# Kernel tuning notes

Hardware: AMD Instinct MI355X
Metric: run time of the kernel (lower is better)

## Reference

```python
import jax, jax.numpy as jnp
import numpy as np

N_NODES = 50000
N_EDGES = 800000
IN_DIM = 128
HID = 128
NUM_CLASSES = 2


def setup_inputs() -> dict:
    key = jax.random.key(0)
    ks = jax.random.split(key, 16)
    inp = {
        "adj_row": jax.random.randint(ks[0], (N_EDGES,), 0, N_NODES),
        "adj_col": jax.random.randint(ks[1], (N_EDGES,), 0, N_NODES),
        "adj_vals": jax.random.uniform(ks[2], (N_EDGES,), dtype=jnp.float32),
        "input_feature": jax.random.normal(ks[3], (N_NODES, IN_DIM), dtype=jnp.float32),
        "graph_indicator": jax.random.randint(ks[4], (N_NODES,), 0, 64),
        # GCN layer params (kaiming-uniform-ish init; zeros bias like the torch module)
        "W1": jax.random.uniform(ks[5], (IN_DIM, HID), jnp.float32, -1, 1) * np.sqrt(6.0 / IN_DIM),
        "b1": jnp.zeros((HID,), jnp.float32),
        "W2": jax.random.uniform(ks[6], (HID, HID), jnp.float32, -1, 1) * np.sqrt(6.0 / HID),
        "b2": jnp.zeros((HID,), jnp.float32),
        "W3": jax.random.uniform(ks[7], (HID, HID), jnp.float32, -1, 1) * np.sqrt(6.0 / HID),
        "b3": jnp.zeros((HID,), jnp.float32),
        # fc params (torch.nn.Linear default init range)
        "fcW1": jax.random.uniform(ks[8], (3 * HID, HID), jnp.float32, -1, 1) / np.sqrt(3 * HID),
        "fcb1": jax.random.uniform(ks[9], (HID,), jnp.float32, -1, 1) / np.sqrt(3 * HID),
        "fcW2": jax.random.uniform(ks[10], (HID, HID // 2), jnp.float32, -1, 1) / np.sqrt(HID),
        "fcb2": jax.random.uniform(ks[11], (HID // 2,), jnp.float32, -1, 1) / np.sqrt(HID),
        "fcW3": jax.random.uniform(ks[12], (HID // 2, NUM_CLASSES), jnp.float32, -1, 1) / np.sqrt(HID // 2),
        "fcb3": jax.random.uniform(ks[13], (NUM_CLASSES,), jnp.float32, -1, 1) / np.sqrt(HID // 2),
    }
    return inp


def _gcn_layer(row, col, vals, x, W, b, n_nodes):
    # support = X @ W  -> dense GEMM
    support = x @ W
    # sparse.mm(A, support): out[i] = sum_{e: row[e]=i} vals[e] * support[col[e]]
    msgs = support[col] * vals[:, None]  # [E, D] gather + scale
    agg = jax.ops.segment_sum(msgs, row, num_segments=n_nodes)
    return agg + b


def reference(adj_row, adj_col, adj_vals, input_feature, graph_indicator,
              W1, b1, W2, b2, W3, b3, fcW1, fcb1, fcW2, fcb2, fcW3, fcb3):
    n = input_feature.shape[0]
    g1 = jax.nn.relu(_gcn_layer(adj_row, adj_col, adj_vals, input_feature, W1, b1, n))
    g2 = jax.nn.relu(_gcn_layer(adj_row, adj_col, adj_vals, g1, W2, b2, n))
    g3 = jax.nn.relu(_gcn_layer(adj_row, adj_col, adj_vals, g2, W3, b3, n))
    feat = jnp.concatenate([g1, g2, g3], axis=1)  # [N, 3*HID]
    h = jax.nn.relu(feat @ fcW1 + fcb1)
    h = jax.nn.relu(h @ fcW2 + fcb2)
    logits = h @ fcW3 + fcb3
    return logits
```

## Files before the change

kernel.cpp:

```cpp
#include <hip/hip_runtime.h>
#include <hip/hip_bf16.h>

#define N_NODES 50000
#define N_EDGES 800000
#define NBK 391
#define BCAP 2560
#define PADSLACK 896

static inline int cdiv(int a, int b) { return (a + b - 1) / b; }

typedef __attribute__((ext_vector_type(8))) short short8;
typedef __attribute__((ext_vector_type(4))) float f32x4;

__device__ __forceinline__ float b2f(unsigned short u) {
    union { unsigned int i; float f; } c;
    c.i = ((unsigned int)u) << 16;
    return c.f;
}
__device__ __forceinline__ unsigned short f2bb(float f) {
    __hip_bfloat16 h = __float2bfloat16(f);
    return *(unsigned short*)&h;
}

__device__ __forceinline__ void pack_one(const float* __restrict__ W,
                                         __hip_bfloat16* __restrict__ out,
                                         int K, int N, int t) {
    int lane = t & 63;
    int kc = (t >> 6) % (K / 32);
    int nt = (t >> 6) / (K / 32);
    int kbase = kc * 32 + (lane >> 4) * 8;
    int col = nt * 16 + (lane & 15);
    __hip_bfloat16* dst = out + (size_t)t * 8;
#pragma unroll
    for (int j = 0; j < 8; ++j)
        dst[j] = __float2bfloat16(W[(size_t)(kbase + j) * N + col]);
}

__global__ __launch_bounds__(256)
void stage1_kernel(const int* __restrict__ row, const int* __restrict__ col,
                   const float* __restrict__ vals, int* __restrict__ bcursor,
                   int2* __restrict__ tmp, int E,
                   const float* __restrict__ x, __hip_bfloat16* __restrict__ support,
                   int M,
                   const float* __restrict__ W1, const float* __restrict__ W2,
                   const float* __restrict__ W3, const float* __restrict__ fcW1,
                   const float* __restrict__ fcW2,
                   __hip_bfloat16* __restrict__ pW2, __hip_bfloat16* __restrict__ pW3,
                   __hip_bfloat16* __restrict__ pfcW1, __hip_bfloat16* __restrict__ pfcW2) {
    __shared__ unsigned short As[64][136];
    __shared__ int hist[NBK];
    __shared__ int base[NBK];
    const int b = blockIdx.x;
    const int tid = threadIdx.x;

    if (b < 196) {
        const int CH = 4096;
        int e0 = b * CH;
        for (int i = tid; i < NBK; i += 256) hist[i] = 0;
        __syncthreads();
        for (int i = tid; i < CH; i += 256) {
            int e = e0 + i;
            if (e < E) atomicAdd(&hist[row[e] >> 7], 1);
        }
        __syncthreads();
        for (int i = tid; i < NBK; i += 256) {
            int c = hist[i];
            base[i] = (c > 0) ? (i * BCAP + atomicAdd(&bcursor[i], c)) : 0;
            hist[i] = 0;
        }
        __syncthreads();
        for (int i = tid; i < CH; i += 256) {
            int e = e0 + i;
            if (e < E) {
                int r = row[e];
                int bk = r >> 7;
                int rk = atomicAdd(&hist[bk], 1);
                tmp[base[bk] + rk] = make_int2(((r & 127) << 16) | col[e],
                                               __float_as_int(vals[e]));
            }
        }
        return;
    }

    if (b < 978) {
        const int wave = tid >> 6;
        const int lane = tid & 63;
        const int ln15 = lane & 15;
        const int quad = lane >> 4;
        const int m0 = (b - 196) * 64;

        short8 bfr[4][2];
#pragma unroll
        for (int kc = 0; kc < 4; ++kc)
#pragma unroll
            for (int h = 0; h < 2; ++h)
#pragma unroll
                for (int j = 0; j < 8; ++j)
                    bfr[kc][h][j] = (short)f2bb(
                        W1[(size_t)(kc * 32 + quad * 8 + j) * 128 + (wave * 2 + h) * 16 + ln15]);

#pragma unroll
        for (int i = 0; i < 4; ++i) {
            int idx = tid + i * 256;
            int r = idx >> 4;
            int c8 = (idx & 15) * 8;
            uint4 pk = {0, 0, 0, 0};
            if (m0 + r < M) {
                const float* src = &x[(size_t)(m0 + r) * 128 + c8];
                float4 a = *(const float4*)src;
                float4 bq = *(const float4*)(src + 4);
                pk.x = f2bb(a.x) | ((unsigned int)f2bb(a.y) << 16);
                pk.y = f2bb(a.z) | ((unsigned int)f2bb(a.w) << 16);
                pk.z = f2bb(bq.x) | ((unsigned int)f2bb(bq.y) << 16);
                pk.w = f2bb(bq.z) | ((unsigned int)f2bb(bq.w) << 16);
            }
            *(uint4*)&As[r][c8] = pk;
        }
        __syncthreads();

        f32x4 acc[4][2];
#pragma unroll
        for (int s = 0; s < 4; ++s)
#pragma unroll
            for (int h = 0; h < 2; ++h) acc[s][h] = (f32x4){0.f, 0.f, 0.f, 0.f};
#pragma unroll
        for (int kc = 0; kc < 4; ++kc) {
            short8 af[4];
#pragma unroll
            for (int s = 0; s < 4; ++s)
                af[s] = *(const short8*)&As[s * 16 + ln15][kc * 32 + quad * 8];
#pragma unroll
            for (int s = 0; s < 4; ++s)
#pragma unroll
                for (int h = 0; h < 2; ++h)
                    acc[s][h] = __builtin_amdgcn_mfma_f32_16x16x32_bf16(
                        af[s], bfr[kc][h], acc[s][h], 0, 0, 0);
        }
#pragma unroll
        for (int s = 0; s < 4; ++s)
#pragma unroll
            for (int h = 0; h < 2; ++h) {
                int cl = (wave * 2 + h) * 16 + ln15;
#pragma unroll
                for (int r = 0; r < 4; ++r) {
                    int rw = m0 + s * 16 + quad * 4 + r;
                    if (rw < M)
                        support[(size_t)rw * 128 + cl] = __float2bfloat16(acc[s][h][r]);
                }
            }
        return;
    }

    int pb = b - 978;
    if (pb < 8)       pack_one(W2,  pW2,  128, 128, pb * 256 + tid);
    else if (pb < 16) pack_one(W3,  pW3,  128, 128, (pb - 8) * 256 + tid);
    else if (pb < 40) pack_one(fcW1, pfcW1, 384, 128, (pb - 16) * 256 + tid);
    else              pack_one(fcW2, pfcW2, 128, 64, (pb - 40) * 256 + tid);
}

__global__ __launch_bounds__(256)
void binB_kernel(const int2* __restrict__ tmp, const int* __restrict__ bcursor,
                 int2* __restrict__ rowrange, int2* __restrict__ epack, int N) {
    int b = blockIdx.x;
    int r0 = b << 7;
    int nr = N - r0; if (nr > 128) nr = 128;
    __shared__ int cnt[128];
    __shared__ int cur[128];
    __shared__ int rpos[128];
    __shared__ int red[256];
    int t = threadIdx.x;
    int partial = 0;
    for (int i = t; i < b; i += 256) partial += bcursor[i];
    red[t] = partial;
    if (t < 128) cnt[t] = 0;
    __syncthreads();
    for (int off = 128; off > 0; off >>= 1) {
        if (t < off) red[t] += red[t + off];
        __syncthreads();
    }
    int slab = b * BCAP;
    int send = slab + bcursor[b];
    for (int i = slab + t; i < send; i += 256)
        atomicAdd(&cnt[tmp[i].x >> 16], 1);
    __syncthreads();
    int rcnt = (t < 128) ? cnt[t] : 0;
    int pc = (rcnt + 7) & ~7;
    if (t < 128) cur[t] = pc;
    __syncthreads();
    for (int off = 1; off < 128; off <<= 1) {
        int u = (t >= off && t < 128) ? cur[t - off] : 0;
        __syncthreads();
        if (t < 128) cur[t] += u;
        __syncthreads();
    }
    int obase = red[0] + b * PADSLACK;
    if (t < 128) {
        int pos = obase + cur[t] - pc;
        rpos[t] = pos;
        cur[t] = pos;
        if (t < nr) rowrange[r0 + t] = make_int2(pos, pos + pc);
    }
    __syncthreads();
    for (int i = slab + t; i < send; i += 256) {
        int2 v = tmp[i];
        int rl = v.x >> 16;
        int c = v.x & 0xffff;
        int pos = atomicAdd(&cur[rl], 1);
        epack[pos] = make_int2(c, v.y);
    }
    if (t < 128) {
        int rc = rcnt;
        int pos = rpos[t];
#pragma unroll 1
        for (int i = pos + rc; i < pos + pc; ++i)
            epack[i] = make_int2(0, 0);
    }
}

__device__ __forceinline__ void accum8(float* acc, long long e, uint4 u) {
    float f = __int_as_float((int)(e >> 32));
    acc[0] += f * b2f((unsigned short)(u.x & 0xffff));
    acc[1] += f * b2f((unsigned short)(u.x >> 16));
    acc[2] += f * b2f((unsigned short)(u.y & 0xffff));
    acc[3] += f * b2f((unsigned short)(u.y >> 16));
    acc[4] += f * b2f((unsigned short)(u.z & 0xffff));
    acc[5] += f * b2f((unsigned short)(u.z >> 16));
    acc[6] += f * b2f((unsigned short)(u.w & 0xffff));
    acc[7] += f * b2f((unsigned short)(u.w >> 16));
}

__device__ __forceinline__ void agg_node(const long long* __restrict__ ep,
                                         const __hip_bfloat16* __restrict__ support,
                                         int p, int end, int g, int j, float* acc) {
#pragma unroll
    for (int k = 0; k < 8; ++k) acc[k] = 0.f;
    long long e0 = 0, e1 = 0;
    uint4 u0 = {0, 0, 0, 0}, u1 = {0, 0, 0, 0};
    bool have = false;
    if (p < end) {
        e0 = ep[p + g];
        e1 = ep[p + 4 + g];
        u0 = *(const uint4*)&support[(size_t)(unsigned int)(e0 & 0xffffffffu) * 128 + j * 8];
        u1 = *(const uint4*)&support[(size_t)(unsigned int)(e1 & 0xffffffffu) * 128 + j * 8];
        p += 8;
        have = true;
    }
    while (p < end) {
        long long f0 = ep[p + g];
        long long f1 = ep[p + 4 + g];
        uint4 w0 = *(const uint4*)&support[(size_t)(unsigned int)(f0 & 0xffffffffu) * 128 + j * 8];
        uint4 w1 = *(const uint4*)&support[(size_t)(unsigned int)(f1 & 0xffffffffu) * 128 + j * 8];
        accum8(acc, e0, u0);
        accum8(acc, e1, u1);
        e0 = f0; u0 = w0; e1 = f1; u1 = w1;
        p += 8;
    }
    if (have) {
        accum8(acc, e0, u0);
        accum8(acc, e1, u1);
    }
#pragma unroll
    for (int k = 0; k < 8; ++k) {
        acc[k] += __shfl_xor(acc[k], 16);
        acc[k] += __shfl_xor(acc[k], 32);
    }
}

__global__ __launch_bounds__(256, 3)
void spmm_gemm_kernel(const int2* __restrict__ rowrange,
                      const int2* __restrict__ epack,
                      const __hip_bfloat16* __restrict__ support,
                      const float* __restrict__ bias,
                      __hip_bfloat16* __restrict__ gout,
                      const __hip_bfloat16* __restrict__ pW,
                      __hip_bfloat16* __restrict__ Cout,
                      int N) {
    __shared__ unsigned short As[64][136];
    const int tid = threadIdx.x;
    const int wv = tid >> 6;
    const int l = tid & 63;
    const int g = l >> 4;
    const int j = l & 15;
    const int m0 = blockIdx.x * 64;
    const long long* ep = (const long long*)epack;
    float4 b0 = *(const float4*)&bias[j * 8];
    float4 b1 = *(const float4*)&bias[j * 8 + 4];

    for (int i = 0; i < 16; ++i) {
        int node = m0 + wv * 16 + i;
        if (node >= N) {
            if (g == 0) *(uint4*)&As[wv * 16 + i][j * 8] = (uint4){0, 0, 0, 0};
            continue;
        }
        int2 rr = rowrange[node];
        float acc[8];
        agg_node(ep, support, rr.x, rr.y, g, j, acc);
        if (g == 0) {
            unsigned int q0 = (unsigned int)f2bb(fmaxf(acc[0] + b0.x, 0.f))
                            | ((unsigned int)f2bb(fmaxf(acc[1] + b0.y, 0.f)) << 16);
            unsigned int q1 = (unsigned int)f2bb(fmaxf(acc[2] + b0.z, 0.f))
                            | ((unsigned int)f2bb(fmaxf(acc[3] + b0.w, 0.f)) << 16);
            unsigned int q2 = (unsigned int)f2bb(fmaxf(acc[4] + b1.x, 0.f))
                            | ((unsigned int)f2bb(fmaxf(acc[5] + b1.y, 0.f)) << 16);
            unsigned int q3 = (unsigned int)f2bb(fmaxf(acc[6] + b1.z, 0.f))
                            | ((unsigned int)f2bb(fmaxf(acc[7] + b1.w, 0.f)) << 16);
            uint4 st = {q0, q1, q2, q3};
            *(uint4*)&As[wv * 16 + i][j * 8] = st;
            *(uint4*)&gout[(size_t)node * 384 + j * 8] = st;
        }
    }
    __syncthreads();

    const int ln15 = l & 15;
    const int quad = l >> 4;
    const int ntw = wv * 2;
    f32x4 acc2[4][2];
#pragma unroll
    for (int s = 0; s < 4; ++s)
#pragma unroll
        for (int h = 0; h < 2; ++h) acc2[s][h] = (f32x4){0.f, 0.f, 0.f, 0.f};
#pragma unroll
    for (int kc = 0; kc < 4; ++kc) {
        short8 af[4];
#pragma unroll
        for (int s = 0; s < 4; ++s)
            af[s] = *(const short8*)&As[s * 16 + ln15][kc * 32 + quad * 8];
        short8 bf[2];
#pragma unroll
        for (int h = 0; h < 2; ++h)
            bf[h] = *(const short8*)&pW[((size_t)((ntw + h) * 4 + kc) * 64 + l) * 8];
#pragma unroll
        for (int s = 0; s < 4; ++s)
#pragma unroll
            for (int h = 0; h < 2; ++h)
                acc2[s][h] = __builtin_amdgcn_mfma_f32_16x16x32_bf16(
                    af[s], bf[h], acc2[s][h], 0, 0, 0);
    }
#pragma unroll
    for (int s = 0; s < 4; ++s)
#pragma unroll
        for (int h = 0; h < 2; ++h) {
            int cl = (ntw + h) * 16 + ln15;
#pragma unroll
            for (int r = 0; r < 4; ++r) {
                int rw = m0 + s * 16 + quad * 4 + r;
                if (rw < N)
                    Cout[(size_t)rw * 128 + cl] = __float2bfloat16(acc2[s][h][r]);
            }
        }
}

__global__ __launch_bounds__(256, 3)
void spmm_fc_kernel(const int2* __restrict__ rowrange,
                    const int2* __restrict__ epack,
                    const __hip_bfloat16* __restrict__ support,
                    const float* __restrict__ bias,
                    const __hip_bfloat16* __restrict__ featb,
                    const __hip_bfloat16* __restrict__ pfcW1,
                    const float* __restrict__ fcb1,
                    const __hip_bfloat16* __restrict__ pfcW2,
                    const float* __restrict__ fcb2,
                    const float* __restrict__ fcW3, const float* __restrict__ fcb3,
                    float* __restrict__ out, int N) {
    __shared__ unsigned short As[64][136];
    __shared__ float w3s[128];
    __shared__ float b3s[2];
    const int tid = threadIdx.x;
    const int wv = tid >> 6;
    const int l = tid & 63;
    const int g = l >> 4;
    const int j = l & 15;
    const int m0 = blockIdx.x * 64;
    const long long* ep = (const long long*)epack;
    if (tid < 128) w3s[tid] = fcW3[tid];
    if (tid < 2) b3s[tid] = fcb3[tid];
    float4 b0 = *(const float4*)&bias[j * 8];
    float4 b1 = *(const float4*)&bias[j * 8 + 4];

    for (int i = 0; i < 16; ++i) {
        int node = m0 + wv * 16 + i;
        if (node >= N) {
            if (g == 0) *(uint4*)&As[wv * 16 + i][j * 8] = (uint4){0, 0, 0, 0};
            continue;
        }
        int2 rr = rowrange[node];
        float acc[8];
        agg_node(ep, support, rr.x, rr.y, g, j, acc);
        if (g == 0) {
            unsigned int q0 = (unsigned int)f2bb(fmaxf(acc[0] + b0.x, 0.f))
                            | ((unsigned int)f2bb(fmaxf(acc[1] + b0.y, 0.f)) << 16);
            unsigned int q1 = (unsigned int)f2bb(fmaxf(acc[2] + b0.z, 0.f))
                            | ((unsigned int)f2bb(fmaxf(acc[3] + b0.w, 0.f)) << 16);
            unsigned int q2 = (unsigned int)f2bb(fmaxf(acc[4] + b1.x, 0.f))
                            | ((unsigned int)f2bb(fmaxf(acc[5] + b1.y, 0.f)) << 16);
            unsigned int q3 = (unsigned int)f2bb(fmaxf(acc[6] + b1.z, 0.f))
                            | ((unsigned int)f2bb(fmaxf(acc[7] + b1.w, 0.f)) << 16);
            uint4 st = {q0, q1, q2, q3};
            *(uint4*)&As[wv * 16 + i][j * 8] = st;
        }
    }
    __syncthreads();

    const int lane = l;
    const int ln15 = lane & 15;
    const int quad = lane >> 4;
    const int wave = wv;
    f32x4 acc[4][2];
#pragma unroll
    for (int s = 0; s < 4; ++s)
#pragma unroll
        for (int h = 0; h < 2; ++h) acc[s][h] = (f32x4){0.f, 0.f, 0.f, 0.f};
#pragma unroll
    for (int step = 0; step < 3; ++step) {
        const int kb = (step == 0) ? 2 : (step - 1);
        if (step != 0) {
            __syncthreads();
#pragma unroll
            for (int i = 0; i < 4; ++i) {
                int idx = tid + i * 256;
                int r = idx >> 4;
                int c8 = (idx & 15) * 8;
                uint4 v = *(const uint4*)&featb[(size_t)(m0 + r) * 384 + kb * 128 + c8];
                *(uint4*)&As[r][c8] = v;
            }
            __syncthreads();
        }
#pragma unroll
        for (int kc = 0; kc < 4; ++kc) {
            short8 af[4];
#pragma unroll
            for (int s = 0; s < 4; ++s)
                af[s] = *(const short8*)&As[s * 16 + ln15][kc * 32 + quad * 8];
            short8 bf[2];
#pragma unroll
            for (int h = 0; h < 2; ++h) {
                int kcg = kb * 4 + kc;
                bf[h] = *(const short8*)&pfcW1[((size_t)((wave * 2 + h) * 12 + kcg) * 64 + lane) * 8];
            }
#pragma unroll
            for (int s = 0; s < 4; ++s)
#pragma unroll
                for (int h = 0; h < 2; ++h)
                    acc[s][h] = __builtin_amdgcn_mfma_f32_16x16x32_bf16(
                        af[s], bf[h], acc[s][h], 0, 0, 0);
        }
    }
    __syncthreads();
#pragma unroll
    for (int s = 0; s < 4; ++s)
#pragma unroll
        for (int h = 0; h < 2; ++h) {
            int col = (wave * 2 + h) * 16 + ln15;
            float bv = fcb1[col];
#pragma unroll
            for (int r = 0; r < 4; ++r) {
                int row = s * 16 + quad * 4 + r;
                As[row][col] = f2bb(fmaxf(acc[s][h][r] + bv, 0.f));
            }
        }
    __syncthreads();

    f32x4 acc2[4];
#pragma unroll
    for (int s = 0; s < 4; ++s) acc2[s] = (f32x4){0.f, 0.f, 0.f, 0.f};
#pragma unroll
    for (int kc = 0; kc < 4; ++kc) {
        short8 af[4];
#pragma unroll
        for (int s = 0; s < 4; ++s)
            af[s] = *(const short8*)&As[s * 16 + ln15][kc * 32 + quad * 8];
        short8 bfw = *(const short8*)&pfcW2[((size_t)(wave * 4 + kc) * 64 + lane) * 8];
#pragma unroll
        for (int s = 0; s < 4; ++s)
            acc2[s] = __builtin_amdgcn_mfma_f32_16x16x32_bf16(af[s], bfw, acc2[s], 0, 0, 0);
    }
    __syncthreads();
    {
        int col2 = wave * 16 + ln15;
        float bv = fcb2[col2];
#pragma unroll
        for (int s = 0; s < 4; ++s)
#pragma unroll
            for (int r = 0; r < 4; ++r) {
                int row = s * 16 + quad * 4 + r;
                As[row][col2] = f2bb(fmaxf(acc2[s][r] + bv, 0.f));
            }
    }
    __syncthreads();

    if (tid < 128) {
        int row = tid >> 1, cls = tid & 1;
        int grow = m0 + row;
        if (grow < N) {
            float a = b3s[cls];
#pragma unroll
            for (int k = 0; k < 64; ++k)
                a += b2f(As[row][k]) * w3s[k * 2 + cls];
            out[(size_t)grow * 2 + cls] = a;
        }
    }
}

extern "C" void kernel_launch(void* const* d_in, const int* in_sizes, int n_in,
                              void* d_out, int out_size, void* d_ws, size_t ws_size,
                              hipStream_t stream) {
    const int*   adj_row  = (const int*)d_in[0];
    const int*   adj_col  = (const int*)d_in[1];
    const float* adj_vals = (const float*)d_in[2];
    const float* x        = (const float*)d_in[3];
    const float* W1   = (const float*)d_in[5];
    const float* b1   = (const float*)d_in[6];
    const float* W2   = (const float*)d_in[7];
    const float* b2   = (const float*)d_in[8];
    const float* W3   = (const float*)d_in[9];
    const float* b3   = (const float*)d_in[10];
    const float* fcW1 = (const float*)d_in[11];
    const float* fcb1 = (const float*)d_in[12];
    const float* fcW2 = (const float*)d_in[13];
    const float* fcb2 = (const float*)d_in[14];
    const float* fcW3 = (const float*)d_in[15];
    const float* fcb3 = (const float*)d_in[16];
    float* out = (float*)d_out;

    const int N = N_NODES, E = N_EDGES;
    const int Mpad = 50048;
    const int EPAD = E + NBK * PADSLACK + 64;

    char* p = (char*)d_ws;
    auto alloc = [&](size_t bytes) {
        char* q = p;
        p += (bytes + 255) & ~(size_t)255;
        return q;
    };
    __hip_bfloat16* featb    = (__hip_bfloat16*)alloc((size_t)Mpad * 384 * 2);
    __hip_bfloat16* supportb = (__hip_bfloat16*)alloc((size_t)Mpad * 128 * 2);
    __hip_bfloat16* supportc = (__hip_bfloat16*)alloc((size_t)Mpad * 128 * 2);
    __hip_bfloat16* pW2   = (__hip_bfloat16*)alloc(16384 * 2);
    __hip_bfloat16* pW3   = (__hip_bfloat16*)alloc(16384 * 2);
    __hip_bfloat16* pfcW1 = (__hip_bfloat16*)alloc(49152 * 2);
    __hip_bfloat16* pfcW2 = (__hip_bfloat16*)alloc(8192 * 2);
    int2*  rowrange  = (int2*)alloc((size_t)(N + 1) * 8);
    int*   bcursor   = (int*)alloc((size_t)NBK * 4);
    int2*  epack     = (int2*)alloc((size_t)EPAD * 8);
    int2*  tmp       = (int2*)alloc((size_t)NBK * BCAP * 8);

    hipMemsetAsync(bcursor, 0, (size_t)NBK * 4, stream);
    stage1_kernel<<<1022, 256, 0, stream>>>(adj_row, adj_col, adj_vals, bcursor, tmp, E,
                                            x, supportb, N,
                                            W1, W2, W3, fcW1, fcW2,
                                            pW2, pW3, pfcW1, pfcW2);
    binB_kernel<<<NBK, 256, 0, stream>>>(tmp, bcursor, rowrange, epack, N);

    const int fgrid = cdiv(N, 64);

    spmm_gemm_kernel<<<fgrid, 256, 0, stream>>>(rowrange, epack, supportb, b1,
                                                featb + 0, pW2, supportc, N);
    spmm_gemm_kernel<<<fgrid, 256, 0, stream>>>(rowrange, epack, supportc, b2,
                                                featb + 128, pW3, supportb, N);
    spmm_fc_kernel<<<fgrid, 256, 0, stream>>>(rowrange, epack, supportb, b3,
                                              featb, pfcW1, fcb1, pfcW2, fcb2,
                                              fcW3, fcb3, out, N);
}
```

Measured before the change: 273.9 us.

## Use 512-thread blocks in fused SpMM kernels, one MFMA tile per wave

The fused aggregation+GEMM kernels now launch 8 waves per 64-node block instead of 4. Each wave aggregates 8 nodes instead of 16 and computes one 16-column output tile instead of two. This raises the number of waves in flight for the latency-bound gather, at the cost of an extra barrier branch and idle waves in the fc2 stage. The fc kernel runs its second layer on only the first four waves. The non-uniform __syncthreads inside the if/else branches is a correctness risk.

```diff
diff --git a/kernel.cpp b/kernel.cpp
--- a/kernel.cpp
+++ b/kernel.cpp
@@ -266,7 +266,7 @@
     }
 }
 
-__global__ __launch_bounds__(256, 3)
+__global__ __launch_bounds__(512, 4)
 void spmm_gemm_kernel(const int2* __restrict__ rowrange,
                       const int2* __restrict__ epack,
                       const __hip_bfloat16* __restrict__ support,
@@ -286,10 +286,10 @@
     float4 b0 = *(const float4*)&bias[j * 8];
     float4 b1 = *(const float4*)&bias[j * 8 + 4];
 
-    for (int i = 0; i < 16; ++i) {
-        int node = m0 + wv * 16 + i;
+    for (int i = 0; i < 8; ++i) {
+        int node = m0 + wv * 8 + i;
         if (node >= N) {
-            if (g == 0) *(uint4*)&As[wv * 16 + i][j * 8] = (uint4){0, 0, 0, 0};
+            if (g == 0) *(uint4*)&As[wv * 8 + i][j * 8] = (uint4){0, 0, 0, 0};
             continue;
         }
         int2 rr = rowrange[node];
@@ -305,52 +305,42 @@
             unsigned int q3 = (unsigned int)f2bb(fmaxf(acc[6] + b1.z, 0.f))
                             | ((unsigned int)f2bb(fmaxf(acc[7] + b1.w, 0.f)) << 16);
             uint4 st = {q0, q1, q2, q3};
-            *(uint4*)&As[wv * 16 + i][j * 8] = st;
-            *(uint4*)&gout[(size_t)node * 384 + j * 8] = st;
+            *(uint4*)&As[wv * 8 + i][j * 8] = st;
+            *(uint4*)&gout[(size_t)(m0 + wv * 8 + i) * 384 + j * 8] = st;
         }
     }
     __syncthreads();
 
     const int ln15 = l & 15;
     const int quad = l >> 4;
-    const int ntw = wv * 2;
-    f32x4 acc2[4][2];
-#pragma unroll
-    for (int s = 0; s < 4; ++s)
-#pragma unroll
-        for (int h = 0; h < 2; ++h) acc2[s][h] = (f32x4){0.f, 0.f, 0.f, 0.f};
+    f32x4 acc2[4];
+#pragma unroll
+    for (int s = 0; s < 4; ++s) acc2[s] = (f32x4){0.f, 0.f, 0.f, 0.f};
 #pragma unroll
     for (int kc = 0; kc < 4; ++kc) {
         short8 af[4];
 #pragma unroll
         for (int s = 0; s < 4; ++s)
             af[s] = *(const short8*)&As[s * 16 + ln15][kc * 32 + quad * 8];
-        short8 bf[2];
-#pragma unroll
-        for (int h = 0; h < 2; ++h)
-            bf[h] = *(const short8*)&pW[((size_t)((ntw + h) * 4 + kc) * 64 + l) * 8];
-#pragma unroll
-        for (int s = 0; s < 4; ++s)
-#pragma unroll
-            for (int h = 0; h < 2; ++h)
-                acc2[s][h] = __builtin_amdgcn_mfma_f32_16x16x32_bf16(
-                    af[s], bf[h], acc2[s][h], 0, 0, 0);
-    }
-#pragma unroll
-    for (int s = 0; s < 4; ++s)
-#pragma unroll
-        for (int h = 0; h < 2; ++h) {
-            int cl = (ntw + h) * 16 + ln15;
+        short8 bf = *(const short8*)&pW[((size_t)(wv * 4 + kc) * 64 + l) * 8];
+#pragma unroll
+        for (int s = 0; s < 4; ++s)
+            acc2[s] = __builtin_amdgcn_mfma_f32_16x16x32_bf16(af[s], bf, acc2[s], 0, 0, 0);
+    }
+    {
+        int cl = wv * 16 + ln15;
+#pragma unroll
+        for (int s = 0; s < 4; ++s)
 #pragma unroll
             for (int r = 0; r < 4; ++r) {
                 int rw = m0 + s * 16 + quad * 4 + r;
                 if (rw < N)
-                    Cout[(size_t)rw * 128 + cl] = __float2bfloat16(acc2[s][h][r]);
-            }
-        }
-}
-
-__global__ __launch_bounds__(256, 3)
+                    Cout[(size_t)rw * 128 + cl] = __float2bfloat16(acc2[s][r]);
+            }
+    }
+}
+
+__global__ __launch_bounds__(512, 4)
 void spmm_fc_kernel(const int2* __restrict__ rowrange,
                     const int2* __restrict__ epack,
                     const __hip_bfloat16* __restrict__ support,
@@ -377,10 +367,10 @@
     float4 b0 = *(const float4*)&bias[j * 8];
     float4 b1 = *(const float4*)&bias[j * 8 + 4];
 
-    for (int i = 0; i < 16; ++i) {
-        int node = m0 + wv * 16 + i;
+    for (int i = 0; i < 8; ++i) {
+        int node = m0 + wv * 8 + i;
         if (node >= N) {
-            if (g == 0) *(uint4*)&As[wv * 16 + i][j * 8] = (uint4){0, 0, 0, 0};
+            if (g == 0) *(uint4*)&As[wv * 8 + i][j * 8] = (uint4){0, 0, 0, 0};
             continue;
         }
         int2 rr = rowrange[node];
@@ -396,28 +386,24 @@
             unsigned int q3 = (unsigned int)f2bb(fmaxf(acc[6] + b1.z, 0.f))
                             | ((unsigned int)f2bb(fmaxf(acc[7] + b1.w, 0.f)) << 16);
             uint4 st = {q0, q1, q2, q3};
-            *(uint4*)&As[wv * 16 + i][j * 8] = st;
-        }
-    }
-    __syncthreads();
-
-    const int lane = l;
-    const int ln15 = lane & 15;
-    const int quad = lane >> 4;
-    const int wave = wv;
-    f32x4 acc[4][2];
-#pragma unroll
-    for (int s = 0; s < 4; ++s)
-#pragma unroll
-        for (int h = 0; h < 2; ++h) acc[s][h] = (f32x4){0.f, 0.f, 0.f, 0.f};
+            *(uint4*)&As[wv * 8 + i][j * 8] = st;
+        }
+    }
+    __syncthreads();
+
+    const int ln15 = l & 15;
+    const int quad = l >> 4;
+    f32x4 acc[4];
+#pragma unroll
+    for (int s = 0; s < 4; ++s) acc[s] = (f32x4){0.f, 0.f, 0.f, 0.f};
 #pragma unroll
     for (int step = 0; step < 3; ++step) {
         const int kb = (step == 0) ? 2 : (step - 1);
         if (step != 0) {
             __syncthreads();
 #pragma unroll
-            for (int i = 0; i < 4; ++i) {
-                int idx = tid + i * 256;
+            for (int i = 0; i < 2; ++i) {
+                int idx = tid + i * 512;
                 int r = idx >> 4;
                 int c8 = (idx & 15) * 8;
                 uint4 v = *(const uint4*)&featb[(size_t)(m0 + r) * 384 + kb * 128 + c8];
@@ -431,52 +417,44 @@
 #pragma unroll
             for (int s = 0; s < 4; ++s)
                 af[s] = *(const short8*)&As[s * 16 + ln15][kc * 32 + quad * 8];
-            short8 bf[2];
-#pragma unroll
-            for (int h = 0; h < 2; ++h) {
-                int kcg = kb * 4 + kc;
-                bf[h] = *(const short8*)&pfcW1[((size_t)((wave * 2 + h) * 12 + kcg) * 64 + lane) * 8];
-            }
+            int kcg = kb * 4 + kc;
+            short8 bf = *(const short8*)&pfcW1[((size_t)(wv * 12 + kcg) * 64 + l) * 8];
 #pragma unroll
             for (int s = 0; s < 4; ++s)
-#pragma unroll
-                for (int h = 0; h < 2; ++h)
-                    acc[s][h] = __builtin_amdgcn_mfma_f32_16x16x32_bf16(
-                        af[s], bf[h], acc[s][h], 0, 0, 0);
-        }
-    }
-    __syncthreads();
-#pragma unroll
-    for (int s = 0; s < 4; ++s)
-#pragma unroll
-        for (int h = 0; h < 2; ++h) {
-            int col = (wave * 2 + h) * 16 + ln15;
-            float bv = fcb1[col];
+                acc[s] = __builtin_amdgcn_mfma_f32_16x16x32_bf16(af[s], bf, acc[s], 0, 0, 0);
+        }
+    }
+    __syncthreads();
+    {
+        int col = wv * 16 + ln15;
+        float bv = fcb1[col];
+#pragma unroll
+        for (int s = 0; s < 4; ++s)
 #pragma unroll
             for (int r = 0; r < 4; ++r) {
                 int row = s * 16 + quad * 4 + r;
-                As[row][col] = f2bb(fmaxf(acc[s][h][r] + bv, 0.f));
-            }
-        }
-    __syncthreads();
-
-    f32x4 acc2[4];
-#pragma unroll
-    for (int s = 0; s < 4; ++s) acc2[s] = (f32x4){0.f, 0.f, 0.f, 0.f};
-#pragma unroll
-    for (int kc = 0; kc < 4; ++kc) {
-        short8 af[4];
-#pragma unroll
-        for (int s = 0; s < 4; ++s)
-            af[s] = *(const short8*)&As[s * 16 + ln15][kc * 32 + quad * 8];
-        short8 bfw = *(const short8*)&pfcW2[((size_t)(wave * 4 + kc) * 64 + lane) * 8];
-#pragma unroll
-        for (int s = 0; s < 4; ++s)
-            acc2[s] = __builtin_amdgcn_mfma_f32_16x16x32_bf16(af[s], bfw, acc2[s], 0, 0, 0);
-    }
-    __syncthreads();
-    {
-        int col2 = wave * 16 + ln15;
+                As[row][col] = f2bb(fmaxf(acc[s][r] + bv, 0.f));
+            }
+    }
+    __syncthreads();
+
+    if (wv < 4) {
+        f32x4 acc2[4];
+#pragma unroll
+        for (int s = 0; s < 4; ++s) acc2[s] = (f32x4){0.f, 0.f, 0.f, 0.f};
+#pragma unroll
+        for (int kc = 0; kc < 4; ++kc) {
+            short8 af[4];
+#pragma unroll
+            for (int s = 0; s < 4; ++s)
+                af[s] = *(const short8*)&As[s * 16 + ln15][kc * 32 + quad * 8];
+            short8 bfw = *(const short8*)&pfcW2[((size_t)(wv * 4 + kc) * 64 + l) * 8];
+#pragma unroll
+            for (int s = 0; s < 4; ++s)
+                acc2[s] = __builtin_amdgcn_mfma_f32_16x16x32_bf16(af[s], bfw, acc2[s], 0, 0, 0);
+        }
+        __syncthreads();
+        int col2 = wv * 16 + ln15;
         float bv = fcb2[col2];
 #pragma unroll
         for (int s = 0; s < 4; ++s)
@@ -485,6 +463,8 @@
                 int row = s * 16 + quad * 4 + r;
                 As[row][col2] = f2bb(fmaxf(acc2[s][r] + bv, 0.f));
             }
+    } else {
+        __syncthreads();
     }
     __syncthreads();
 
@@ -553,11 +533,11 @@
 
     const int fgrid = cdiv(N, 64);
 
-    spmm_gemm_kernel<<<fgrid, 256, 0, stream>>>(rowrange, epack, supportb, b1,
+    spmm_gemm_kernel<<<fgrid, 512, 0, stream>>>(rowrange, epack, supportb, b1,
                                                 featb + 0, pW2, supportc, N);
-    spmm_gemm_kernel<<<fgrid, 256, 0, stream>>>(rowrange, epack, supportc, b2,
+    spmm_gemm_kernel<<<fgrid, 512, 0, stream>>>(rowrange, epack, supportc, b2,
                                                 featb + 128, pW3, supportb, N);
-    spmm_fc_kernel<<<fgrid, 256, 0, stream>>>(rowrange, epack, supportb, b3,
+    spmm_fc_kernel<<<fgrid, 512, 0, stream>>>(rowrange, epack, supportb, b3,
                                               featb, pfcW1, fcb1, pfcW2, fcb2,
                                               fcW3, fcb3, out, N);
 }
```

After: 280.4 us. +2.4%, slower.
